# Kernel optimization log

Measured on AMD Instinct MI355X. Metric: run time of the kernel, lower is better.

The kernel has to match this reference:

```python
import jax, jax.numpy as jnp
import numpy as np

B, C, CI, H, W = 4, 256, 128, 48, 48
EPS = 1e-5  # BatchNorm2d default eps


def _make_bn(k, n, c):
    kg, kb, km, kv = jax.random.split(k, 4)
    gamma = 1.0 + 0.1 * jax.random.normal(kg, (n, c), jnp.float32)
    beta = 0.1 * jax.random.normal(kb, (n, c), jnp.float32)
    mean = 0.1 * jax.random.normal(km, (n, c), jnp.float32)
    var = 0.5 + jax.random.uniform(kv, (n, c), jnp.float32)
    return jnp.stack([gamma, beta, mean, var], axis=1)  # [n, 4, c]


def setup_inputs() -> dict:
    key = jax.random.key(0)
    ks = jax.random.split(key, 8)
    x1 = jax.random.normal(ks[0], (B, C, H, W), jnp.float32)
    x2 = jax.random.normal(ks[1], (B, C, H, W), jnp.float32)
    bn_pre = _make_bn(ks[2], 4, C)                       # g1, g2, theta, phi pre-BN
    w_pre = 0.05 * jax.random.normal(ks[3], (4, CI, C), jnp.float32)
    b_pre = 0.01 * jax.random.normal(ks[4], (4, CI), jnp.float32)
    w_post = 0.05 * jax.random.normal(ks[5], (2, C, CI), jnp.float32)  # W1, W2 convs
    b_post = 0.01 * jax.random.normal(ks[6], (2, C), jnp.float32)
    bn_post = _make_bn(ks[7], 2, C)                      # W1, W2 post-BN
    return dict(x1=x1, x2=x2, bn_pre=bn_pre, w_pre=w_pre, b_pre=b_pre,
                w_post=w_post, b_post=b_post, bn_post=bn_post)


def _bn(x, p):
    # eval-mode BatchNorm2d: p = [gamma, beta, mean, var], each [C]
    gamma, beta, mean, var = p[0], p[1], p[2], p[3]
    scale = (gamma / jnp.sqrt(var + EPS))[:, None, None]
    return (x - mean[:, None, None]) * scale + beta[:, None, None]


def reference(x1, x2, bn_pre, w_pre, b_pre, w_post, b_post, bn_post):
    Bsz, _, Hh, Ww = x1.shape
    N = Hh * Ww

    def pre(x, i):  # BN -> 1x1 conv -> flatten to [B, CI, N]
        h = _bn(x, bn_pre[i])
        y = jnp.einsum('oc,bchw->bohw', w_pre[i], h) + b_pre[i][None, :, None, None]
        return y.reshape(Bsz, -1, N)

    g11 = pre(x1, 0)   # g1(x1)
    g21 = pre(x2, 1)   # g2(x2)
    th1 = pre(x1, 2)   # theta(x1)
    ph1 = pre(x2, 3)   # phi(x2)

    e_time = jnp.einsum('bcn,bdn->bcd', th1, ph1)    # [B, CI, CI]  (theta @ phi^T)
    e_space = jnp.einsum('bcn,bcm->bnm', th1, ph1)   # [B, N, N]    (theta^T @ phi)

    et1s = jax.nn.softmax(e_time, axis=-1)                          # energy_time_1s
    et2s = jax.nn.softmax(jnp.swapaxes(e_time, 1, 2), axis=-1)      # energy_time_2s
    es2s = jax.nn.softmax(e_space, axis=-2)                         # energy_space_2s
    es1s = jax.nn.softmax(jnp.swapaxes(e_space, 1, 2), axis=-2)     # energy_space_1s

    y1 = jnp.einsum('bcd,bdn,bnm->bcm', et2s, g11, es2s).reshape(Bsz, -1, Hh, Ww)
    y2 = jnp.einsum('bcd,bdn,bnm->bcm', et1s, g21, es1s).reshape(Bsz, -1, Hh, Ww)

    def post(y, i):  # 1x1 conv -> BN
        h = jnp.einsum('oc,bchw->bohw', w_post[i], y) + b_post[i][None, :, None, None]
        return _bn(h, bn_post[i])

    return (x1 + post(y1, 0), x2 + post(y2, 1))
```

## Files before the change

kernel.cpp:

```cpp
#include <hip/hip_runtime.h>
#include <hip/hip_bf16.h>


#define N_PIX 2304
#define NB 4

typedef __attribute__((ext_vector_type(8))) short bf16x8;
typedef __attribute__((ext_vector_type(4))) float f32x4;

__device__ __forceinline__ short f2bf(float f) {
  unsigned u = __float_as_uint(f);
  unsigned r = (u + 0x7fffu + ((u >> 16) & 1u)) >> 16;
  return (short)r;
}
__device__ __forceinline__ float bf2f(short s) {
  return __uint_as_float(((unsigned)(unsigned short)s) << 16);
}
__device__ __forceinline__ int swz(int row, int kc) {
  return kc ^ ((row ^ (row >> 3)) & 7);
}
__device__ __forceinline__ unsigned pk2(short a, short b) {
  return (unsigned)(unsigned short)a | ((unsigned)(unsigned short)b << 16);
}


struct GArgs {
  const short *a0, *a1, *al0, *al1;
  const short *b0, *b1, *bl0, *bl1;
  long sa, sb, sal, sbl;
  int lda, ldb, lal, lbl;
  int K, ksplit, kchunk;
  int bt0, bt1;
  void *o0, *o1; long so;
  void *p0, *p1; long sp;
  void *q0, *q1; long sq;
  void *u0, *u1; long su;
  const float *aux0, *aux1; long saux;
  const float *res0, *res1; long sres;
};

template <int EPI, int SPLIT>
__global__ __launch_bounds__(256) void mgemm(GArgs g) {
  int z = blockIdx.z;
  int pb = z / g.ksplit, ks = z - pb * g.ksplit;
  int sel = pb >> 2, batch = pb & 3;
  const short* A = (sel ? g.a1 : g.a0) + (long)batch * g.sa;
  const short* B = (sel ? g.b1 : g.b0) + (long)batch * g.sb;
  const short* Al = nullptr; const short* Bl = nullptr;
  if (SPLIT) {
    Al = (sel ? g.al1 : g.al0) + (long)batch * g.sal;
    Bl = (sel ? g.bl1 : g.bl0) + (long)batch * g.sbl;
  }
  int bt = sel ? g.bt1 : g.bt0;
  int k0 = ks * g.kchunk, k1 = k0 + g.kchunk;
  int m0 = blockIdx.y << 7, n0 = blockIdx.x << 7;

  __shared__ short As[128 * 64];
  __shared__ short Bs[128 * 64];
  __shared__ short Als[SPLIT ? 128 * 64 : 8];
  __shared__ short Bls[SPLIT ? 128 * 64 : 8];

  int t = threadIdx.x;
  int lane = t & 63, wid = t >> 6;
  int wm = (wid >> 1) << 6, wn = (wid & 1) << 6;
  int l15 = lane & 15, lg = lane >> 4;

  f32x4 acc[4][4];
  #pragma unroll
  for (int i = 0; i < 4; ++i)
    #pragma unroll
    for (int j = 0; j < 4; ++j) acc[i][j] = (f32x4){0.f, 0.f, 0.f, 0.f};

  for (int kt = k0; kt < k1; kt += 64) {
    __syncthreads();
    #pragma unroll
    for (int i = 0; i < 4; ++i) {
      int ch = t + (i << 8);
      int row = ch >> 3, kc = ch & 7;
      int di = (row << 6) + (swz(row, kc) << 3);
      *(bf16x8*)&As[di] = *(const bf16x8*)&A[(long)(m0 + row) * g.lda + kt + (kc << 3)];
      if (SPLIT)
        *(bf16x8*)&Als[di] = *(const bf16x8*)&Al[(long)(m0 + row) * g.lal + kt + (kc << 3)];
    }
    if (!bt) {
      #pragma unroll
      for (int i = 0; i < 4; ++i) {
        int ch = t + (i << 8);
        int row = ch >> 3, kc = ch & 7;
        int di = (row << 6) + (swz(row, kc) << 3);
        *(bf16x8*)&Bs[di] = *(const bf16x8*)&B[(long)(n0 + row) * g.ldb + kt + (kc << 3)];
        if (SPLIT)
          *(bf16x8*)&Bls[di] = *(const bf16x8*)&Bl[(long)(n0 + row) * g.lbl + kt + (kc << 3)];
      }
    } else {
      #pragma unroll
      for (int i = 0; i < 4; ++i) {
        int ch = t + (i << 8);
        int nc = ch & 15, kk = ch >> 4;
        bf16x8 ld = *(const bf16x8*)&B[(long)(kt + kk) * g.ldb + n0 + (nc << 3)];
        int kc = kk >> 3, w = kk & 7;
        #pragma unroll
        for (int e = 0; e < 8; ++e) {
          int rn = (nc << 3) + e;
          Bs[(rn << 6) + (swz(rn, kc) << 3) + w] = ld[e];
        }
      }
    }
    __syncthreads();
    #pragma unroll
    for (int ksub = 0; ksub < 2; ++ksub) {
      int kb = (ksub << 2) + lg;
      bf16x8 ah[4], bh[4], alv[4], blv[4];
      #pragma unroll
      for (int i = 0; i < 4; ++i) {
        int ra = wm + (i << 4) + l15;
        int rb = wn + (i << 4) + l15;
        ah[i] = *(const bf16x8*)&As[(ra << 6) + (swz(ra, kb) << 3)];
        bh[i] = *(const bf16x8*)&Bs[(rb << 6) + (swz(rb, kb) << 3)];
        if (SPLIT) {
          alv[i] = *(const bf16x8*)&Als[(ra << 6) + (swz(ra, kb) << 3)];
          blv[i] = *(const bf16x8*)&Bls[(rb << 6) + (swz(rb, kb) << 3)];
        }
      }
      #pragma unroll
      for (int i = 0; i < 4; ++i)
        #pragma unroll
        for (int j = 0; j < 4; ++j) {
          if (SPLIT) {
            acc[i][j] = __builtin_amdgcn_mfma_f32_16x16x32_bf16(alv[i], bh[j], acc[i][j], 0, 0, 0);
            acc[i][j] = __builtin_amdgcn_mfma_f32_16x16x32_bf16(ah[i], blv[j], acc[i][j], 0, 0, 0);
          }
          acc[i][j] = __builtin_amdgcn_mfma_f32_16x16x32_bf16(ah[i], bh[j], acc[i][j], 0, 0, 0);
        }
    }
  }

  #pragma unroll
  for (int j = 0; j < 4; ++j) {
    int col = n0 + wn + (j << 4) + l15;
    float sc = 1.f;
    if (EPI == 4) {
      const float* S = (sel ? g.aux1 : g.aux0) + (long)batch * g.saux;
      sc = 1.0f / S[col];
    }
    #pragma unroll
    for (int i = 0; i < 4; ++i) {
      int row0 = m0 + wm + (i << 4) + (lg << 2);
      if (EPI == 0) {
        const float* bias = (sel ? g.aux1 : g.aux0);
        short* FTB_ = (short*)(sel ? g.q1 : g.q0) + (long)batch * g.sq;
        float v[4]; short hh[4];
        #pragma unroll
        for (int r = 0; r < 4; ++r) { v[r] = acc[i][j][r] + bias[row0 + r]; hh[r] = f2bf(v[r]); }
        uint2 pk; pk.x = pk2(hh[0], hh[1]); pk.y = pk2(hh[2], hh[3]);
        *(uint2*)&FTB_[(long)col * 256 + row0] = pk;
        if (row0 >= 128) {
          short* FB_  = (short*)(sel ? g.o1 : g.o0) + (long)batch * g.so;
          short* FLO_ = (short*)(sel ? g.p1 : g.p0) + (long)batch * g.sp;
          short* FTL_ = (short*)(sel ? g.u1 : g.u0) + (long)batch * g.su;
          short ll[4];
          #pragma unroll
          for (int r = 0; r < 4; ++r) {
            ll[r] = f2bf(v[r] - bf2f(hh[r]));
            FB_[(long)(row0 - 128 + r) * N_PIX + col] = hh[r];
            FLO_[(long)(row0 - 128 + r) * N_PIX + col] = ll[r];
          }
          uint2 pl; pl.x = pk2(ll[0], ll[1]); pl.y = pk2(ll[2], ll[3]);
          *(uint2*)&FTL_[(long)col * 128 + (row0 - 128)] = pl;
        }
      } else if (EPI == 1) {
        float* ET_ = (float*)g.o0 + (long)batch * g.so;
        #pragma unroll
        for (int r = 0; r < 4; ++r) atomicAdd(&ET_[(long)(row0 + r) * 128 + col], acc[i][j][r]);
      } else if (EPI == 2) {
        short* PT_ = (short*)g.o0 + (long)batch * g.so;
        short hh[4];
        #pragma unroll
        for (int r = 0; r < 4; ++r) hh[r] = f2bf(__expf(acc[i][j][r]));
        uint2 pk; pk.x = pk2(hh[0], hh[1]); pk.y = pk2(hh[2], hh[3]);
        *(uint2*)&PT_[(long)col * N_PIX + row0] = pk;
      } else if (EPI == 3) {
        short* AB_ = (short*)(sel ? g.o1 : g.o0) + (long)batch * g.so;
        #pragma unroll
        for (int r = 0; r < 4; ++r) AB_[(long)(row0 + r) * N_PIX + col] = f2bf(acc[i][j][r]);
      } else if (EPI == 4) {
        short* YT_ = (short*)(sel ? g.o1 : g.o0) + (long)batch * g.so;
        short hh[4];
        #pragma unroll
        for (int r = 0; r < 4; ++r) hh[r] = f2bf(acc[i][j][r] * sc);
        uint2 pk; pk.x = pk2(hh[0], hh[1]); pk.y = pk2(hh[2], hh[3]);
        *(uint2*)&YT_[(long)col * 128 + row0] = pk;
      } else {
        float* O_ = (float*)(sel ? g.o1 : g.o0) + (long)batch * g.so;
        const float* bias = (sel ? g.aux1 : g.aux0);
        const float* R_ = (sel ? g.res1 : g.res0) + (long)batch * g.sres;
        #pragma unroll
        for (int r = 0; r < 4; ++r)
          O_[(long)(row0 + r) * N_PIX + col] =
              acc[i][j][r] + bias[row0 + r] + R_[(long)(row0 + r) * N_PIX + col];
      }
    }
  }
}


__global__ __launch_bounds__(256) void xcast(const float* __restrict__ x1,
                                             const float* __restrict__ x2,
                                             short* __restrict__ XH, short* __restrict__ XL) {
  __shared__ float tile[32][33];
  int z = blockIdx.z; int sel = z >> 2, b = z & 3;
  const float* X = (sel ? x2 : x1) + (long)b * 256 * N_PIX;
  long obase = ((long)(sel * 4 + b)) * N_PIX * 256;
  int n0 = blockIdx.x << 5, c0 = blockIdx.y << 5;
  int tx = threadIdx.x & 31, ty = threadIdx.x >> 5;
  #pragma unroll
  for (int i = 0; i < 4; ++i)
    tile[ty + (i << 3)][tx] = X[(long)(c0 + ty + (i << 3)) * N_PIX + n0 + tx];
  __syncthreads();
  #pragma unroll
  for (int i = 0; i < 4; ++i) {
    int n = n0 + ty + (i << 3);
    float v = tile[tx][ty + (i << 3)];
    short h = f2bf(v);
    XH[obase + (long)n * 256 + c0 + tx] = h;
    XL[obase + (long)n * 256 + c0 + tx] = f2bf(v - bf2f(h));
  }
}

__global__ __launch_bounds__(256) void fold_pre(const float* __restrict__ bn,
                                                const float* __restrict__ w,
                                                const float* __restrict__ b,
                                                short* __restrict__ WH, short* __restrict__ WL,
                                                float* __restrict__ Bc) {
  int blk = blockIdx.x;
  int xsel = blk >> 8, row = blk & 255;
  int i = (row < 128) ? xsel : (2 + xsel);
  int o = row & 127;
  int c = threadIdx.x;
  const float* bni = bn + i * 1024;
  float gm = bni[c], be = bni[256 + c], mn = bni[512 + c], vr = bni[768 + c];
  float s = gm * rsqrtf(vr + 1e-5f);
  float tb = be - mn * s;
  float wv = w[(i * 128 + o) * 256 + c];
  float val = wv * s;
  short h = f2bf(val);
  long idx = (long)(xsel * 256 + row) * 256 + c;
  WH[idx] = h;
  WL[idx] = f2bf(val - bf2f(h));
  __shared__ float red[256];
  red[c] = wv * tb;
  __syncthreads();
  for (int off = 128; off > 0; off >>= 1) {
    if (c < off) red[c] += red[c + off];
    __syncthreads();
  }
  if (c == 0) Bc[xsel * 256 + row] = b[i * 128 + o] + red[0];
}

__global__ __launch_bounds__(128) void fold_post(const float* __restrict__ bn,
                                                 const float* __restrict__ w,
                                                 const float* __restrict__ b,
                                                 short* __restrict__ WB, float* __restrict__ Bc) {
  int blk = blockIdx.x;
  int i = blk >> 8, o = blk & 255;
  const float* bni = bn + i * 1024;
  float s = bni[o] * rsqrtf(bni[768 + o] + 1e-5f);
  int c = threadIdx.x;
  long idx = (long)(i * 256 + o) * 128 + c;
  WB[idx] = f2bf(w[idx] * s);
  if (c == 0) Bc[i * 256 + o] = b[i * 256 + o] * s + bni[256 + o] - bni[512 + o] * s;
}

__global__ __launch_bounds__(128) void et_softmax(const float* __restrict__ Et,
                                                  short* __restrict__ MB) {
  __shared__ float Es[128 * 128];
  int b = blockIdx.x, t = threadIdx.x;
  const float* E = Et + (long)b * 16384;
  for (int i = t; i < 16384; i += 128) Es[i] = E[i];
  __syncthreads();
  short* M1 = MB + (long)b * 16384;
  short* M2 = MB + (long)(4 + b) * 16384;
  float rm = -1e30f;
  for (int j = 0; j < 128; ++j) rm = fmaxf(rm, Es[t * 128 + j]);
  float rs = 0.f;
  for (int j = 0; j < 128; ++j) rs += __expf(Es[t * 128 + j] - rm);
  float ri = 1.0f / rs;
  for (int j = 0; j < 128; ++j) M2[t * 128 + j] = f2bf(__expf(Es[t * 128 + j] - rm) * ri);
  float cm = -1e30f;
  for (int d = 0; d < 128; ++d) cm = fmaxf(cm, Es[d * 128 + t]);
  float cs = 0.f;
  for (int d = 0; d < 128; ++d) cs += __expf(Es[d * 128 + t] - cm);
  float ci = 1.0f / cs;
  for (int d = 0; d < 128; ++d) M1[t * 128 + d] = f2bf(__expf(Es[d * 128 + t] - cm) * ci);
}

__global__ __launch_bounds__(256) void rowsum(const short* __restrict__ P, float* __restrict__ S) {
  long row = blockIdx.x;
  const short* p = P + row * N_PIX;
  int t = threadIdx.x;
  float s = 0.f;
  for (int c = t; c < 288; c += 256) {
    bf16x8 v = *(const bf16x8*)&p[c << 3];
    #pragma unroll
    for (int e = 0; e < 8; ++e) s += bf2f(v[e]);
  }
  #pragma unroll
  for (int off = 32; off > 0; off >>= 1) s += __shfl_down(s, off, 64);
  __shared__ float red[4];
  if ((t & 63) == 0) red[t >> 6] = s;
  __syncthreads();
  if (t == 0) S[row] = red[0] + red[1] + red[2] + red[3];
}

__global__ __launch_bounds__(256) void colsum(const short* __restrict__ PT, float* __restrict__ S) {
  int b = blockIdx.z;
  int c = (blockIdx.x << 8) + threadIdx.x;
  int r0 = blockIdx.y << 7;
  const short* p = PT + (long)b * N_PIX * N_PIX + (long)r0 * N_PIX + c;
  float s = 0.f;
  for (int r = 0; r < 128; ++r) s += bf2f(p[(long)r * N_PIX]);
  atomicAdd(&S[b * N_PIX + c], s);
}

extern "C" void kernel_launch(void* const* d_in, const int* in_sizes, int n_in,
                              void* d_out, int out_size, void* d_ws, size_t ws_size,
                              hipStream_t stream) {
  const float* x1 = (const float*)d_in[0];
  const float* x2 = (const float*)d_in[1];
  const float* bn_pre = (const float*)d_in[2];
  const float* w_pre = (const float*)d_in[3];
  const float* b_pre = (const float*)d_in[4];
  const float* w_post = (const float*)d_in[5];
  const float* b_post = (const float*)d_in[6];
  const float* bn_post = (const float*)d_in[7];
  float* out = (float*)d_out;

  char* W = (char*)d_ws;
  float* BPRE  = (float*)(W + 0);
  float* BPOST = (float*)(W + 2048);
  float* CS    = (float*)(W + 4096);
  float* RS    = (float*)(W + 40960);
  float* ET    = (float*)(W + 77824);
  short* WPREH = (short*)(W + 339968);
  short* WPREL = (short*)(W + 602112);
  short* WPOSTB= (short*)(W + 864256);
  short* MB    = (short*)(W + 995328);
  short* XTH   = (short*)(W + 1257472);
  short* XTL   = (short*)(W + 10694656);
  short* FB    = (short*)(W + 20131840);
  short* FLO   = (short*)(W + 24850432);
  short* FTB   = (short*)(W + 29569024);
  short* FTLO  = (short*)(W + 39006208);
  short* AB    = (short*)(W + 43724800);
  short* YT    = (short*)(W + 48443392);
  short* PT    = (short*)(W + 53161984);

  hipMemsetAsync(ET, 0, 262144, stream);
  hipMemsetAsync(RS, 0, 36864, stream);
  xcast<<<dim3(72, 8, 8), 256, 0, stream>>>(x1, x2, XTH, XTL);
  fold_pre<<<512, 256, 0, stream>>>(bn_pre, w_pre, b_pre, WPREH, WPREL, BPRE);
  fold_post<<<512, 128, 0, stream>>>(bn_post, w_post, b_post, WPOSTB, BPOST);

  { GArgs g{};
    g.a0 = WPREH; g.a1 = WPREH + 65536; g.al0 = WPREL; g.al1 = WPREL + 65536;
    g.sa = 0; g.sal = 0; g.lda = 256; g.lal = 256;
    g.b0 = XTH; g.b1 = XTH + 4L * 2304 * 256; g.bl0 = XTL; g.bl1 = XTL + 4L * 2304 * 256;
    g.sb = 2304L * 256; g.sbl = 2304L * 256; g.ldb = 256; g.lbl = 256;
    g.K = 256; g.ksplit = 1; g.kchunk = 256; g.bt0 = 0; g.bt1 = 0;
    g.o0 = FB; g.o1 = FB + 4L * 128 * 2304; g.so = 128L * 2304;
    g.p0 = FLO; g.p1 = FLO + 4L * 128 * 2304; g.sp = 128L * 2304;
    g.q0 = FTB; g.q1 = FTB + 4L * 2304 * 256; g.sq = 2304L * 256;
    g.u0 = FTLO; g.u1 = FTLO + 4L * 2304 * 128; g.su = 2304L * 128;
    g.aux0 = BPRE; g.aux1 = BPRE + 256; g.saux = 0;
    mgemm<0, 1><<<dim3(18, 2, 8), 256, 0, stream>>>(g); }

  { GArgs g{};
    g.a0 = g.a1 = FB; g.al0 = g.al1 = FLO;
    g.sa = g.sal = 128L * 2304; g.lda = g.lal = 2304;
    g.b0 = g.b1 = FB + 4L * 128 * 2304; g.bl0 = g.bl1 = FLO + 4L * 128 * 2304;
    g.sb = g.sbl = 128L * 2304; g.ldb = g.lbl = 2304;
    g.K = 2304; g.ksplit = 12; g.kchunk = 192; g.bt0 = 0; g.bt1 = 0;
    g.o0 = g.o1 = ET; g.so = 16384;
    mgemm<1, 1><<<dim3(1, 1, 48), 256, 0, stream>>>(g); }

  et_softmax<<<4, 128, 0, stream>>>(ET, MB);

  { GArgs g{};
    g.a0 = g.a1 = FTB + 128; g.al0 = g.al1 = FTLO;
    g.sa = 2304L * 256; g.sal = 2304L * 128; g.lda = 256; g.lal = 128;
    g.b0 = g.b1 = FTB + 4L * 2304 * 256 + 128; g.bl0 = g.bl1 = FTLO + 4L * 2304 * 128;
    g.sb = 2304L * 256; g.sbl = 2304L * 128; g.ldb = 256; g.lbl = 128;
    g.K = 128; g.ksplit = 1; g.kchunk = 128; g.bt0 = 0; g.bt1 = 0;
    g.o0 = g.o1 = PT; g.so = (long)2304 * 2304;
    mgemm<2, 1><<<dim3(18, 18, 4), 256, 0, stream>>>(g); }

  rowsum<<<9216, 256, 0, stream>>>(PT, CS);
  colsum<<<dim3(9, 18, 4), 256, 0, stream>>>(PT, RS);

  { GArgs g{};
    g.a0 = MB; g.a1 = MB + 4 * 16384; g.sa = 16384; g.lda = 128;
    g.b0 = FTB; g.b1 = FTB + 4L * 2304 * 256; g.sb = 2304L * 256; g.ldb = 256;
    g.K = 128; g.ksplit = 1; g.kchunk = 128; g.bt0 = 0; g.bt1 = 0;
    g.o0 = AB; g.o1 = AB + 4L * 128 * 2304; g.so = 128L * 2304;
    mgemm<3, 0><<<dim3(18, 1, 8), 256, 0, stream>>>(g); }

  { GArgs g{};
    g.a0 = AB; g.a1 = AB + 4L * 128 * 2304; g.sa = 128L * 2304; g.lda = 2304;
    g.b0 = g.b1 = PT; g.sb = (long)2304 * 2304; g.ldb = 2304;
    g.K = 2304; g.ksplit = 1; g.kchunk = 2304; g.bt0 = 0; g.bt1 = 1;
    g.o0 = YT; g.o1 = YT + 4L * 2304 * 128; g.so = 2304L * 128;
    g.aux0 = CS; g.aux1 = RS; g.saux = 2304;
    mgemm<4, 0><<<dim3(18, 1, 8), 256, 0, stream>>>(g); }

  { GArgs g{};
    g.a0 = WPOSTB; g.a1 = WPOSTB + 32768; g.sa = 0; g.lda = 128;
    g.b0 = YT; g.b1 = YT + 4L * 2304 * 128; g.sb = 2304L * 128; g.ldb = 128;
    g.K = 128; g.ksplit = 1; g.kchunk = 128; g.bt0 = 0; g.bt1 = 0;
    g.o0 = out; g.o1 = out + 4L * 256 * 2304; g.so = 256L * 2304;
    g.aux0 = BPOST; g.aux1 = BPOST + 256; g.saux = 0;
    g.res0 = x1; g.res1 = x2; g.sres = 256L * 2304;
    mgemm<5, 0><<<dim3(18, 2, 8), 256, 0, stream>>>(g); }
}
```

Baseline: 284.8 us.

## Fuse softmax row/col sums into exp GEMM epilogue and split-K the PV GEMM

Computes the spatial softmax row and column sums inside the exp-producing GEMM epilogue using wave shuffles and atomics, which removes the separate rowsum and colsum passes over the 2304x2304 probability matrix. The large PV GEMM, which previously launched only 144 blocks, now uses a 6-way split-K that accumulates into an fp32 buffer with atomics. A new yreduce kernel then applies the normalisation and converts to bf16. The energy-time GEMM split is also raised from 12 to 36. In exchange this adds atomic traffic, an extra 9 MB memset and fp32 buffer round-trip, and reduction order that is not deterministic.

Result: slower. 439.3 us (+54.3%).

```diff
diff --git a/kernel.cpp b/kernel.cpp
--- a/kernel.cpp
+++ b/kernel.cpp
@@ -135,14 +135,15 @@
     }
   }
 
+  float rsacc[16];
+  if (EPI == 2) {
+    #pragma unroll
+    for (int q = 0; q < 16; ++q) rsacc[q] = 0.f;
+  }
   #pragma unroll
   for (int j = 0; j < 4; ++j) {
     int col = n0 + wn + (j << 4) + l15;
-    float sc = 1.f;
-    if (EPI == 4) {
-      const float* S = (sel ? g.aux1 : g.aux0) + (long)batch * g.saux;
-      sc = 1.0f / S[col];
-    }
+    float csacc = 0.f;
     #pragma unroll
     for (int i = 0; i < 4; ++i) {
       int row0 = m0 + wm + (i << 4) + (lg << 2);
@@ -176,20 +177,22 @@
         short* PT_ = (short*)g.o0 + (long)batch * g.so;
         short hh[4];
         #pragma unroll
-        for (int r = 0; r < 4; ++r) hh[r] = f2bf(__expf(acc[i][j][r]));
+        for (int r = 0; r < 4; ++r) {
+          float ev = __expf(acc[i][j][r]);
+          hh[r] = f2bf(ev);
+          csacc += ev;
+          rsacc[(i << 2) + r] += ev;
+        }
         uint2 pk; pk.x = pk2(hh[0], hh[1]); pk.y = pk2(hh[2], hh[3]);
         *(uint2*)&PT_[(long)col * N_PIX + row0] = pk;
       } else if (EPI == 3) {
         short* AB_ = (short*)(sel ? g.o1 : g.o0) + (long)batch * g.so;
         #pragma unroll
         for (int r = 0; r < 4; ++r) AB_[(long)(row0 + r) * N_PIX + col] = f2bf(acc[i][j][r]);
-      } else if (EPI == 4) {
-        short* YT_ = (short*)(sel ? g.o1 : g.o0) + (long)batch * g.so;
-        short hh[4];
-        #pragma unroll
-        for (int r = 0; r < 4; ++r) hh[r] = f2bf(acc[i][j][r] * sc);
-        uint2 pk; pk.x = pk2(hh[0], hh[1]); pk.y = pk2(hh[2], hh[3]);
-        *(uint2*)&YT_[(long)col * 128 + row0] = pk;
+      } else if (EPI == 6) {
+        float* YTF_ = (float*)(sel ? g.o1 : g.o0) + (long)batch * g.so;
+        #pragma unroll
+        for (int r = 0; r < 4; ++r) atomicAdd(&YTF_[(long)col * 128 + row0 + r], acc[i][j][r]);
       } else {
         float* O_ = (float*)(sel ? g.o1 : g.o0) + (long)batch * g.so;
         const float* bias = (sel ? g.aux1 : g.aux0);
@@ -200,6 +203,28 @@
               acc[i][j][r] + bias[row0 + r] + R_[(long)(row0 + r) * N_PIX + col];
       }
     }
+    if (EPI == 2) {
+      csacc += __shfl_xor(csacc, 16, 64);
+      csacc += __shfl_xor(csacc, 32, 64);
+      if (lg == 0) {
+        float* CSb = (float*)g.p0 + (long)batch * N_PIX;
+        atomicAdd(&CSb[col], csacc);
+      }
+    }
+  }
+  if (EPI == 2) {
+    float* RSb = (float*)g.q0 + (long)batch * N_PIX;
+    #pragma unroll
+    for (int i = 0; i < 4; ++i)
+      #pragma unroll
+      for (int r = 0; r < 4; ++r) {
+        float v = rsacc[(i << 2) + r];
+        v += __shfl_xor(v, 1, 64);
+        v += __shfl_xor(v, 2, 64);
+        v += __shfl_xor(v, 4, 64);
+        v += __shfl_xor(v, 8, 64);
+        if (l15 == 0) atomicAdd(&RSb[m0 + wm + (i << 4) + (lg << 2) + r], v);
+      }
   }
 }
 
@@ -294,32 +319,25 @@
   for (int d = 0; d < 128; ++d) M1[t * 128 + d] = f2bf(__expf(Es[d * 128 + t] - cm) * ci);
 }
 
-__global__ __launch_bounds__(256) void rowsum(const short* __restrict__ P, float* __restrict__ S) {
-  long row = blockIdx.x;
-  const short* p = P + row * N_PIX;
-  int t = threadIdx.x;
-  float s = 0.f;
-  for (int c = t; c < 288; c += 256) {
-    bf16x8 v = *(const bf16x8*)&p[c << 3];
-    #pragma unroll
-    for (int e = 0; e < 8; ++e) s += bf2f(v[e]);
-  }
-  #pragma unroll
-  for (int off = 32; off > 0; off >>= 1) s += __shfl_down(s, off, 64);
-  __shared__ float red[4];
-  if ((t & 63) == 0) red[t >> 6] = s;
-  __syncthreads();
-  if (t == 0) S[row] = red[0] + red[1] + red[2] + red[3];
-}
-
-__global__ __launch_bounds__(256) void colsum(const short* __restrict__ PT, float* __restrict__ S) {
-  int b = blockIdx.z;
-  int c = (blockIdx.x << 8) + threadIdx.x;
-  int r0 = blockIdx.y << 7;
-  const short* p = PT + (long)b * N_PIX * N_PIX + (long)r0 * N_PIX + c;
-  float s = 0.f;
-  for (int r = 0; r < 128; ++r) s += bf2f(p[(long)r * N_PIX]);
-  atomicAdd(&S[b * N_PIX + c], s);
+__global__ __launch_bounds__(256) void yreduce(const float* __restrict__ YTF,
+                                               const float* __restrict__ CS,
+                                               const float* __restrict__ RS,
+                                               short* __restrict__ YT) {
+  long idx = ((long)blockIdx.x * 256 + threadIdx.x) << 3;
+  long z = idx / 294912;
+  long rem = idx - z * 294912;
+  int col = (int)(rem >> 7);
+  int sel = (int)(z >> 2), b = (int)(z & 3);
+  const float* S = sel ? RS : CS;
+  float inv = 1.0f / S[b * N_PIX + col];
+  float4 v0 = *(const float4*)&YTF[idx];
+  float4 v1 = *(const float4*)&YTF[idx + 4];
+  bf16x8 o;
+  o[0] = f2bf(v0.x * inv); o[1] = f2bf(v0.y * inv);
+  o[2] = f2bf(v0.z * inv); o[3] = f2bf(v0.w * inv);
+  o[4] = f2bf(v1.x * inv); o[5] = f2bf(v1.y * inv);
+  o[6] = f2bf(v1.z * inv); o[7] = f2bf(v1.w * inv);
+  *(bf16x8*)&YT[idx] = o;
 }
 
 extern "C" void kernel_launch(void* const* d_in, const int* in_sizes, int n_in,
@@ -354,9 +372,12 @@
   short* AB    = (short*)(W + 43724800);
   short* YT    = (short*)(W + 48443392);
   short* PT    = (short*)(W + 53161984);
+  float* YTF   = (float*)(W + 95629312);
 
   hipMemsetAsync(ET, 0, 262144, stream);
+  hipMemsetAsync(CS, 0, 36864, stream);
   hipMemsetAsync(RS, 0, 36864, stream);
+  hipMemsetAsync(YTF, 0, 9437184, stream);
   xcast<<<dim3(72, 8, 8), 256, 0, stream>>>(x1, x2, XTH, XTL);
   fold_pre<<<512, 256, 0, stream>>>(bn_pre, w_pre, b_pre, WPREH, WPREL, BPRE);
   fold_post<<<512, 128, 0, stream>>>(bn_post, w_post, b_post, WPOSTB, BPOST);
@@ -379,9 +400,9 @@
     g.sa = g.sal = 128L * 2304; g.lda = g.lal = 2304;
     g.b0 = g.b1 = FB + 4L * 128 * 2304; g.bl0 = g.bl1 = FLO + 4L * 128 * 2304;
     g.sb = g.sbl = 128L * 2304; g.ldb = g.lbl = 2304;
-    g.K = 2304; g.ksplit = 12; g.kchunk = 192; g.bt0 = 0; g.bt1 = 0;
+    g.K = 2304; g.ksplit = 36; g.kchunk = 64; g.bt0 = 0; g.bt1 = 0;
     g.o0 = g.o1 = ET; g.so = 16384;
-    mgemm<1, 1><<<dim3(1, 1, 48), 256, 0, stream>>>(g); }
+    mgemm<1, 1><<<dim3(1, 1, 144), 256, 0, stream>>>(g); }
 
   et_softmax<<<4, 128, 0, stream>>>(ET, MB);
 
@@ -392,10 +413,8 @@
     g.sb = 2304L * 256; g.sbl = 2304L * 128; g.ldb = 256; g.lbl = 128;
     g.K = 128; g.ksplit = 1; g.kchunk = 128; g.bt0 = 0; g.bt1 = 0;
     g.o0 = g.o1 = PT; g.so = (long)2304 * 2304;
+    g.p0 = CS; g.q0 = RS;
     mgemm<2, 1><<<dim3(18, 18, 4), 256, 0, stream>>>(g); }
-
-  rowsum<<<9216, 256, 0, stream>>>(PT, CS);
-  colsum<<<dim3(9, 18, 4), 256, 0, stream>>>(PT, RS);
 
   { GArgs g{};
     g.a0 = MB; g.a1 = MB + 4 * 16384; g.sa = 16384; g.lda = 128;
@@ -407,10 +426,11 @@
   { GArgs g{};
     g.a0 = AB; g.a1 = AB + 4L * 128 * 2304; g.sa = 128L * 2304; g.lda = 2304;
     g.b0 = g.b1 = PT; g.sb = (long)2304 * 2304; g.ldb = 2304;
-    g.K = 2304; g.ksplit = 1; g.kchunk = 2304; g.bt0 = 0; g.bt1 = 1;
-    g.o0 = YT; g.o1 = YT + 4L * 2304 * 128; g.so = 2304L * 128;
-    g.aux0 = CS; g.aux1 = RS; g.saux = 2304;
-    mgemm<4, 0><<<dim3(18, 1, 8), 256, 0, stream>>>(g); }
+    g.K = 2304; g.ksplit = 6; g.kchunk = 384; g.bt0 = 0; g.bt1 = 1;
+    g.o0 = YTF; g.o1 = YTF + 4L * 2304 * 128; g.so = 2304L * 128;
+    mgemm<6, 0><<<dim3(18, 1, 48), 256, 0, stream>>>(g); }
+
+  yreduce<<<1152, 256, 0, stream>>>(YTF, CS, RS, YT);
 
   { GArgs g{};
     g.a0 = WPOSTB; g.a1 = WPOSTB + 32768; g.sa = 0; g.lda = 128;
```
